# Kernel optimization log

Hardware: AMD Instinct MI355X
Metric: run time of the kernel (lower is better)

Reference implementation:

```python
import jax, jax.numpy as jnp
import numpy as np

BN_EPS = 1e-5


def _pixel_shuffle(t, r):
    # torch F.pixel_shuffle: [B, C*r^2, H, W] -> [B, C, H*r, W*r]
    B, Cr2, H, W = t.shape
    C = Cr2 // (r * r)
    t = t.reshape(B, C, r, r, H, W)
    t = t.transpose(0, 1, 4, 2, 5, 3)  # B, C, H, r, W, r
    return t.reshape(B, C, H * r, W * r)


def _upsample_bilinear(x, s):
    # F.interpolate(scale_factor=s, mode='bilinear', align_corners=False)
    B, C, H, W = x.shape

    def axis(n_in):
        n_out = n_in * s
        c = (jnp.arange(n_out, dtype=x.dtype) + 0.5) / s - 0.5
        c = jnp.clip(c, 0.0, n_in - 1)
        i0 = jnp.floor(c).astype(jnp.int32)
        i1 = jnp.minimum(i0 + 1, n_in - 1)
        w = c - i0.astype(x.dtype)
        return i0, i1, w

    y0, y1, wy = axis(H)
    x0, x1, wx = axis(W)
    rows = x[:, :, y0, :] * (1.0 - wy)[None, None, :, None] + x[:, :, y1, :] * wy[None, None, :, None]
    out = rows[:, :, :, x0] * (1.0 - wx)[None, None, None, :] + rows[:, :, :, x1] * wx[None, None, None, :]
    return out


def _grid_sample(x, grid):
    # F.grid_sample bilinear, padding_mode='zeros', align_corners=False
    # x: [B,C,H,W], grid: [B,Ho,Wo,2] with (gx, gy) in [-1,1]
    B, C, H, W = x.shape
    gx, gy = grid[..., 0], grid[..., 1]
    ix = ((gx + 1.0) * W - 1.0) * 0.5
    iy = ((gy + 1.0) * H - 1.0) * 0.5
    ix0 = jnp.floor(ix).astype(jnp.int32)
    iy0 = jnp.floor(iy).astype(jnp.int32)
    ix1, iy1 = ix0 + 1, iy0 + 1
    wx1 = ix - ix0.astype(x.dtype)
    wy1 = iy - iy0.astype(x.dtype)
    wx0, wy0 = 1.0 - wx1, 1.0 - wy1

    xf = x.reshape(B, C, H * W)

    def gather(iy_, ix_):
        valid = ((iy_ >= 0) & (iy_ < H) & (ix_ >= 0) & (ix_ < W)).astype(x.dtype)
        idx = jnp.clip(iy_, 0, H - 1) * W + jnp.clip(ix_, 0, W - 1)  # [B,Ho,Wo]
        flat = idx.reshape(B, 1, -1)
        v = jnp.take_along_axis(xf, jnp.broadcast_to(flat, (B, C, flat.shape[-1])), axis=2)
        return v.reshape(B, C, *idx.shape[1:]) * valid[:, None]

    out = (gather(iy0, ix0) * (wy0 * wx0)[:, None]
           + gather(iy0, ix1) * (wy0 * wx1)[:, None]
           + gather(iy1, ix0) * (wy1 * wx0)[:, None]
           + gather(iy1, ix1) * (wy1 * wx1)[:, None])
    return out


def _conv1x1(x, w, b=None):
    y = jnp.einsum('bchw,oc->bohw', x, w)
    if b is not None:
        y = y + b[None, :, None, None]
    return y


def _forward(x, offset_w, offset_b, mask_w, mask_b, conv_w, bn_gamma, bn_beta, bn_mean, bn_var, s):
    B, C, H, W = x.shape
    x_up = _upsample_bilinear(x, s)
    offset = _conv1x1(x, offset_w, offset_b)              # [B, 2*s*s, H, W]
    mask = jax.nn.sigmoid(_conv1x1(x, mask_w, mask_b))    # [B, s*s, H, W]
    offset = _pixel_shuffle(offset, s)                    # [B, 2, H*s, W*s]
    mask = _pixel_shuffle(mask, s)                        # [B, 1, H*s, W*s]
    Hs, Ws = H * s, W * s
    gy = jnp.linspace(-1.0, 1.0, Hs, dtype=x.dtype)
    gx = jnp.linspace(-1.0, 1.0, Ws, dtype=x.dtype)
    GX, GY = jnp.meshgrid(gx, gy)                         # 'xy': GX[h,w]=gx[w], GY[h,w]=gy[h]
    base_grid = jnp.stack((GX, GY), axis=-1)              # [Hs, Ws, 2]
    grid = base_grid[None] + offset.transpose(0, 2, 3, 1)
    sampled = _grid_sample(x_up, grid)
    out = sampled * mask
    y = _conv1x1(out, conv_w)
    y = (y - bn_mean[None, :, None, None]) * jax.lax.rsqrt(bn_var[None, :, None, None] + BN_EPS)
    y = y * bn_gamma[None, :, None, None] + bn_beta[None, :, None, None]
    return y * jax.nn.sigmoid(y)  # SiLU


def setup_inputs() -> dict:
    key = jax.random.key(0)
    ks = jax.random.split(key, 8)
    B, C, H, W, s = 16, 64, 80, 80, 2
    f = jnp.float32
    x = jax.random.normal(ks[0], (B, C, H, W), f)
    offset_w = jax.random.normal(ks[1], (2 * s * s, C), f) * 0.05
    offset_b = jax.random.normal(ks[2], (2 * s * s,), f) * 0.05
    mask_w = jax.random.normal(ks[3], (s * s, C), f) * 0.1
    mask_b = jnp.zeros((s * s,), f)
    conv_w = jax.random.normal(ks[4], (C, C), f) * (1.0 / np.sqrt(C))
    bn_gamma = jnp.ones((C,), f)
    bn_beta = jnp.zeros((C,), f)
    bn_mean = jax.random.normal(ks[5], (C,), f) * 0.1
    bn_var = jax.random.uniform(ks[6], (C,), f, 0.5, 1.5)
    return {"x": x, "offset_w": offset_w, "offset_b": offset_b, "mask_w": mask_w,
            "mask_b": mask_b, "conv_w": conv_w, "bn_gamma": bn_gamma, "bn_beta": bn_beta,
            "bn_mean": bn_mean, "bn_var": bn_var, "scale": 2}


def reference(x, offset_w, offset_b, mask_w, mask_b, conv_w, bn_gamma, bn_beta, bn_mean, bn_var, scale):
    return _forward(x, offset_w, offset_b, mask_w, mask_b, conv_w, bn_gamma, bn_beta, bn_mean, bn_var, scale)
```

## Files before the change

kernel.cpp:

```cpp
#include <hip/hip_runtime.h>

typedef unsigned short ushort_t;
typedef __attribute__((ext_vector_type(8))) short bf16x8;
typedef __attribute__((ext_vector_type(4))) float f32x4;

__device__ __forceinline__ float bf2f(ushort_t u) {
    union { unsigned int i; float f; } v; v.i = ((unsigned int)u) << 16; return v.f;
}
__device__ __forceinline__ ushort_t f2bf(float f) {
    union { float f; unsigned int i; } v; v.f = f;
    unsigned int r = v.i + 0x7FFFu + ((v.i >> 16) & 1u);
    return (ushort_t)(r >> 16);
}

#define BB 16
#define CC 64
#define HH 80
#define WW 80
#define HS 160
#define WS 160
#define HW (HH*WW)
#define HWS (HS*WS)

__global__ void prep_params(const float* __restrict__ offset_w,
                            const float* __restrict__ offset_b,
                            const float* __restrict__ mask_w,
                            const float* __restrict__ mask_b,
                            const float* __restrict__ conv_w,
                            const float* __restrict__ gamma,
                            const float* __restrict__ beta,
                            const float* __restrict__ mean,
                            const float* __restrict__ var,
                            float* __restrict__ wmat, float* __restrict__ wbias,
                            ushort_t* __restrict__ cwBf,
                            float* __restrict__ bnA, float* __restrict__ bnB) {
    int t = threadIdx.x;
    for (int i = t; i < 12 * 64; i += 256) {
        int ch = i >> 6, c = i & 63;
        wmat[i] = ch < 8 ? offset_w[ch * 64 + c] : mask_w[(ch - 8) * 64 + c];
    }
    if (t < 12) wbias[t] = t < 8 ? offset_b[t] : mask_b[t - 8];
    for (int i = t; i < 64 * 64; i += 256) cwBf[i] = f2bf(conv_w[i]);
    if (t < 64) {
        float A = gamma[t] * rsqrtf(var[t] + 1e-5f);
        bnA[t] = A;
        bnB[t] = beta[t] - mean[t] * A;
    }
}

__global__ __launch_bounds__(256) void prep_x(const float* __restrict__ x,
                                              const float* __restrict__ wmat,
                                              const float* __restrict__ wbias,
                                              ushort_t* __restrict__ xT,
                                              float* __restrict__ offs) {
    __shared__ float sX[64 * 65];
    int t = threadIdx.x;
    int tile = blockIdx.x;
    int b = tile / 100;
    int hw0 = (tile - b * 100) * 64;
#pragma unroll
    for (int k = 0; k < 16; ++k) {
        int e = k * 256 + t;
        int c = e >> 6, j = e & 63;
        sX[j * 65 + c] = x[((b * CC + c) * HW) + hw0 + j];
    }
    __syncthreads();
#pragma unroll
    for (int k = 0; k < 16; ++k) {
        int e = k * 256 + t;
        int j = e >> 6, c = e & 63;
        xT[((size_t)(b * HW) + hw0 + j) * CC + c] = f2bf(sX[j * 65 + c]);
    }
    int px = t & 63;
    int chunk = __builtin_amdgcn_readfirstlane(t >> 6);
    int ch0 = chunk * 3;
    const float* w0 = wmat + (ch0 + 0) * 64;
    const float* w1 = wmat + (ch0 + 1) * 64;
    const float* w2 = wmat + (ch0 + 2) * 64;
    float a0 = 0.f, a1 = 0.f, a2 = 0.f;
#pragma unroll 4
    for (int c = 0; c < 64; ++c) {
        float v = sX[px * 65 + c];
        a0 += v * w0[c];
        a1 += v * w1[c];
        a2 += v * w2[c];
    }
    a0 += wbias[ch0 + 0];
    a1 += wbias[ch0 + 1];
    a2 += wbias[ch0 + 2];
    if (ch0 + 0 >= 8) a0 = 1.0f / (1.0f + __expf(-a0));
    if (ch0 + 1 >= 8) a1 = 1.0f / (1.0f + __expf(-a1));
    if (ch0 + 2 >= 8) a2 = 1.0f / (1.0f + __expf(-a2));
    float* op = offs + (size_t)(b * HW + hw0 + px) * 12;
    op[ch0 + 0] = a0;
    op[ch0 + 1] = a1;
    op[ch0 + 2] = a2;
}

#define ACC3(w, k, val) { float _v = (val); \
    w[0] += (k) == 0 ? _v : 0.f; w[1] += (k) == 1 ? _v : 0.f; w[2] += (k) == 2 ? _v : 0.f; }

__device__ __forceinline__ void axis_taps(float pos, int& base, float w[3]) {
    float f = floorf(pos); int u0 = (int)f; float g1 = pos - f;
    w[0] = w[1] = w[2] = 0.f;
    bool v0 = (u0 >= 0) & (u0 < 160);
    bool v1 = (u0 + 1 >= 0) & (u0 + 1 < 160);
    float cc0 = 0.f, cc1 = 0.f; int ca0 = 0, ca1 = 0;
    if (v0) { cc0 = fminf(fmaxf((float)u0 * 0.5f - 0.25f, 0.f), 79.f); ca0 = (int)floorf(cc0); }
    if (v1) { cc1 = fminf(fmaxf((float)(u0 + 1) * 0.5f - 0.25f, 0.f), 79.f); ca1 = (int)floorf(cc1); }
    int first = v0 ? ca0 : (v1 ? ca1 : 0);
    base = min(first, 77);
    if (v0) {
        float wv = cc0 - (float)ca0; int c1 = min(ca0 + 1, 79);
        int k0 = ca0 - base, k1 = c1 - base;
        ACC3(w, k0, (1.f - g1) * (1.f - wv));
        ACC3(w, k1, (1.f - g1) * wv);
    }
    if (v1) {
        float wv = cc1 - (float)ca1; int c1 = min(ca1 + 1, 79);
        int k0 = ca1 - base, k1 = c1 - base;
        ACC3(w, k0, g1 * (1.f - wv));
        ACC3(w, k1, g1 * wv);
    }
}

__global__ __launch_bounds__(256) void dysample_main(const ushort_t* __restrict__ xT,
                                                     const float* __restrict__ offs,
                                                     const ushort_t* __restrict__ cwBf,
                                                     const float* __restrict__ bnA,
                                                     const float* __restrict__ bnB,
                                                     float* __restrict__ out) {
    __shared__ float sTap[64 * 8];
    __shared__ ushort_t S[64 * 72];
    int t = threadIdx.x;
    int lane = t & 63;
    int wave = __builtin_amdgcn_readfirstlane(t >> 6);
    int quad = lane >> 4, nrow = lane & 15;
    int b = blockIdx.y;
    int pix0 = blockIdx.x * 64;

    const ushort_t* wp = cwBf + (wave * 16 + nrow) * 64 + quad * 8;
    bf16x8 af0 = *(const bf16x8*)(wp);
    bf16x8 af1 = *(const bf16x8*)(wp + 32);
    int coutD = wave * 16 + quad * 4;
    float bnAv[4], bnBv[4];
#pragma unroll
    for (int j = 0; j < 4; ++j) { bnAv[j] = bnA[coutD + j]; bnBv[j] = bnB[coutD + j]; }

    if (t < 64) {
        int pix = pix0 + t;
        int ho = pix / WS, wo = pix - ho * WS;
        int h = ho >> 1, w = wo >> 1, r = ((ho & 1) << 1) | (wo & 1);
        const float* op = offs + (size_t)((b * HW) + h * WW + w) * 12;
        float ox = op[r], oy = op[4 + r], mk = op[8 + r];
        float ix = (float)wo * (160.0f / 159.0f) - 0.5f + 80.0f * ox;
        float iy = (float)ho * (160.0f / 159.0f) - 0.5f + 80.0f * oy;
        int cb, rb; float cw[3], rw[3];
        axis_taps(ix, cb, cw);
        axis_taps(iy, rb, rw);
        sTap[t * 8 + 0] = __int_as_float(cb | (rb << 16));
        sTap[t * 8 + 1] = cw[0]; sTap[t * 8 + 2] = cw[1]; sTap[t * 8 + 3] = cw[2];
        sTap[t * 8 + 4] = rw[0]; sTap[t * 8 + 5] = rw[1]; sTap[t * 8 + 6] = rw[2];
        sTap[t * 8 + 7] = mk;
    }
    __syncthreads();

    const ushort_t* xb = xT + (size_t)b * HW * CC;
#pragma unroll 2
    for (int i = 0; i < 16; ++i) {
        int px = wave * 16 + i;
        f32x4 t0 = *(const f32x4*)(sTap + px * 8);
        f32x4 t1 = *(const f32x4*)(sTap + px * 8 + 4);
        int bits = __float_as_int(t0.x);
        int cb = bits & 0xffff, rb = bits >> 16;
        const ushort_t* p0 = xb + (rb * WW + cb) * CC + lane;
        float acc = 0.f;
#pragma unroll
        for (int rr = 0; rr < 3; ++rr) {
            const ushort_t* pr = p0 + rr * (WW * CC);
            float v0 = bf2f(pr[0]);
            float v1 = bf2f(pr[64]);
            float v2 = bf2f(pr[128]);
            float rowa = t0.y * v0 + t0.z * v1 + t0.w * v2;
            float rwv = (rr == 0) ? t1.x : ((rr == 1) ? t1.y : t1.z);
            acc += rwv * rowa;
        }
        S[px * 72 + lane] = f2bf(acc * t1.w);
    }
    __syncthreads();

    f32x4 acc4[4];
#pragma unroll
    for (int n = 0; n < 4; ++n) acc4[n] = (f32x4){0.f, 0.f, 0.f, 0.f};
#pragma unroll
    for (int n = 0; n < 4; ++n) {
        const ushort_t* sp = S + (n * 16 + nrow) * 72 + quad * 8;
        bf16x8 b0 = *(const bf16x8*)(sp);
        bf16x8 b1 = *(const bf16x8*)(sp + 32);
        acc4[n] = __builtin_amdgcn_mfma_f32_16x16x32_bf16(af0, b0, acc4[n], 0, 0, 0);
        acc4[n] = __builtin_amdgcn_mfma_f32_16x16x32_bf16(af1, b1, acc4[n], 0, 0, 0);
    }

    size_t ob = (size_t)b * CC * HWS;
#pragma unroll
    for (int n = 0; n < 4; ++n) {
        int pix = pix0 + n * 16 + nrow;
#pragma unroll
        for (int j = 0; j < 4; ++j) {
            float y = acc4[n][j] * bnAv[j] + bnBv[j];
            float s = y / (1.0f + __expf(-y));
            out[ob + (size_t)(coutD + j) * HWS + pix] = s;
        }
    }
}

extern "C" void kernel_launch(void* const* d_in, const int* in_sizes, int n_in,
                              void* d_out, int out_size, void* d_ws, size_t ws_size,
                              hipStream_t stream) {
    const float* x        = (const float*)d_in[0];
    const float* offset_w = (const float*)d_in[1];
    const float* offset_b = (const float*)d_in[2];
    const float* mask_w   = (const float*)d_in[3];
    const float* mask_b   = (const float*)d_in[4];
    const float* conv_w   = (const float*)d_in[5];
    const float* bn_gamma = (const float*)d_in[6];
    const float* bn_beta  = (const float*)d_in[7];
    const float* bn_mean  = (const float*)d_in[8];
    const float* bn_var   = (const float*)d_in[9];

    char* ws = (char*)d_ws;
    size_t off = 0;
    ushort_t* xT   = (ushort_t*)(ws + off); off += (size_t)BB * HW * CC * 2;
    float*    offs = (float*)(ws + off);    off += (size_t)BB * HW * 12 * 4;
    ushort_t* cwBf = (ushort_t*)(ws + off); off += 64 * 64 * 2;
    float*    wmat = (float*)(ws + off);    off += 12 * 64 * 4;
    float*    wbias= (float*)(ws + off);    off += 64;
    float*    bnA  = (float*)(ws + off);    off += 64 * 4;
    float*    bnB  = (float*)(ws + off);    off += 64 * 4;

    prep_params<<<1, 256, 0, stream>>>(offset_w, offset_b, mask_w, mask_b, conv_w,
                                       bn_gamma, bn_beta, bn_mean, bn_var,
                                       wmat, wbias, cwBf, bnA, bnB);
    prep_x<<<BB * (HW / 64), 256, 0, stream>>>(x, wmat, wbias, xT, offs);
    dysample_main<<<dim3(HWS / 64, BB), 256, 0, stream>>>(xT, offs, cwBf, bnA, bnB,
                                                          (float*)d_out);
}
```

Before: 189.9 us.

## Fold parameter prep into consumer kernels and vectorize transpose loads/stores

Removes the single-block prep_params launch. Its work moves into the consumers: prep_x reads the offset and mask weights directly, and dysample_main converts conv weights to bf16 and computes the BN scale and shift per block. prep_x now uses float4 global loads and 4-wide bf16 stores for the NCHW-to-NHWC transpose, and the offset fetch in dysample_main uses vector loads. This saves a kernel launch and its serialization, at the cost of redundant per-block weight conversion and more scattered LDS writes.

```diff
diff --git a/kernel.cpp b/kernel.cpp
--- a/kernel.cpp
+++ b/kernel.cpp
@@ -2,6 +2,7 @@
 
 typedef unsigned short ushort_t;
 typedef __attribute__((ext_vector_type(8))) short bf16x8;
+typedef __attribute__((ext_vector_type(4))) unsigned short u16x4;
 typedef __attribute__((ext_vector_type(4))) float f32x4;
 
 __device__ __forceinline__ float bf2f(ushort_t u) {
@@ -12,6 +13,7 @@
     unsigned int r = v.i + 0x7FFFu + ((v.i >> 16) & 1u);
     return (ushort_t)(r >> 16);
 }
+__device__ __forceinline__ short f2bs(float f) { return (short)f2bf(f); }
 
 #define BB 16
 #define CC 64
@@ -22,35 +24,11 @@
 #define HW (HH*WW)
 #define HWS (HS*WS)
 
-__global__ void prep_params(const float* __restrict__ offset_w,
-                            const float* __restrict__ offset_b,
-                            const float* __restrict__ mask_w,
-                            const float* __restrict__ mask_b,
-                            const float* __restrict__ conv_w,
-                            const float* __restrict__ gamma,
-                            const float* __restrict__ beta,
-                            const float* __restrict__ mean,
-                            const float* __restrict__ var,
-                            float* __restrict__ wmat, float* __restrict__ wbias,
-                            ushort_t* __restrict__ cwBf,
-                            float* __restrict__ bnA, float* __restrict__ bnB) {
-    int t = threadIdx.x;
-    for (int i = t; i < 12 * 64; i += 256) {
-        int ch = i >> 6, c = i & 63;
-        wmat[i] = ch < 8 ? offset_w[ch * 64 + c] : mask_w[(ch - 8) * 64 + c];
-    }
-    if (t < 12) wbias[t] = t < 8 ? offset_b[t] : mask_b[t - 8];
-    for (int i = t; i < 64 * 64; i += 256) cwBf[i] = f2bf(conv_w[i]);
-    if (t < 64) {
-        float A = gamma[t] * rsqrtf(var[t] + 1e-5f);
-        bnA[t] = A;
-        bnB[t] = beta[t] - mean[t] * A;
-    }
-}
-
 __global__ __launch_bounds__(256) void prep_x(const float* __restrict__ x,
-                                              const float* __restrict__ wmat,
-                                              const float* __restrict__ wbias,
+                                              const float* __restrict__ offset_w,
+                                              const float* __restrict__ offset_b,
+                                              const float* __restrict__ mask_w,
+                                              const float* __restrict__ mask_b,
                                               ushort_t* __restrict__ xT,
                                               float* __restrict__ offs) {
     __shared__ float sX[64 * 65];
@@ -58,26 +36,43 @@
     int tile = blockIdx.x;
     int b = tile / 100;
     int hw0 = (tile - b * 100) * 64;
-#pragma unroll
-    for (int k = 0; k < 16; ++k) {
-        int e = k * 256 + t;
-        int c = e >> 6, j = e & 63;
-        sX[j * 65 + c] = x[((b * CC + c) * HW) + hw0 + j];
+    const float* xb = x + (size_t)b * CC * HW + hw0;
+
+#pragma unroll
+    for (int k = 0; k < 4; ++k) {
+        int idx = k * 256 + t;
+        int c = idx >> 4;
+        int j4 = (idx & 15) << 2;
+        f32x4 v = *(const f32x4*)(xb + c * HW + j4);
+        sX[(j4 + 0) * 65 + c] = v.x;
+        sX[(j4 + 1) * 65 + c] = v.y;
+        sX[(j4 + 2) * 65 + c] = v.z;
+        sX[(j4 + 3) * 65 + c] = v.w;
     }
     __syncthreads();
-#pragma unroll
-    for (int k = 0; k < 16; ++k) {
-        int e = k * 256 + t;
-        int j = e >> 6, c = e & 63;
-        xT[((size_t)(b * HW) + hw0 + j) * CC + c] = f2bf(sX[j * 65 + c]);
-    }
+
+#pragma unroll
+    for (int k = 0; k < 4; ++k) {
+        int idx = k * 256 + t;
+        int px = idx >> 4;
+        int c4 = (idx & 15) << 2;
+        u16x4 u;
+        u.x = f2bf(sX[px * 65 + c4 + 0]);
+        u.y = f2bf(sX[px * 65 + c4 + 1]);
+        u.z = f2bf(sX[px * 65 + c4 + 2]);
+        u.w = f2bf(sX[px * 65 + c4 + 3]);
+        *(u16x4*)(xT + ((size_t)(b * HW) + hw0 + px) * CC + c4) = u;
+    }
+
     int px = t & 63;
     int chunk = __builtin_amdgcn_readfirstlane(t >> 6);
     int ch0 = chunk * 3;
-    const float* w0 = wmat + (ch0 + 0) * 64;
-    const float* w1 = wmat + (ch0 + 1) * 64;
-    const float* w2 = wmat + (ch0 + 2) * 64;
-    float a0 = 0.f, a1 = 0.f, a2 = 0.f;
+    const float* w0 = (ch0 + 0) < 8 ? offset_w + (ch0 + 0) * 64 : mask_w + (ch0 - 8) * 64;
+    const float* w1 = (ch0 + 1) < 8 ? offset_w + (ch0 + 1) * 64 : mask_w + (ch0 - 7) * 64;
+    const float* w2 = (ch0 + 2) < 8 ? offset_w + (ch0 + 2) * 64 : mask_w + (ch0 - 6) * 64;
+    float a0 = (ch0 + 0) < 8 ? offset_b[ch0 + 0] : mask_b[ch0 - 8];
+    float a1 = (ch0 + 1) < 8 ? offset_b[ch0 + 1] : mask_b[ch0 - 7];
+    float a2 = (ch0 + 2) < 8 ? offset_b[ch0 + 2] : mask_b[ch0 - 6];
 #pragma unroll 4
     for (int c = 0; c < 64; ++c) {
         float v = sX[px * 65 + c];
@@ -85,9 +80,6 @@
         a1 += v * w1[c];
         a2 += v * w2[c];
     }
-    a0 += wbias[ch0 + 0];
-    a1 += wbias[ch0 + 1];
-    a2 += wbias[ch0 + 2];
     if (ch0 + 0 >= 8) a0 = 1.0f / (1.0f + __expf(-a0));
     if (ch0 + 1 >= 8) a1 = 1.0f / (1.0f + __expf(-a1));
     if (ch0 + 2 >= 8) a2 = 1.0f / (1.0f + __expf(-a2));
@@ -124,14 +116,22 @@
     }
 }
 
+__device__ __forceinline__ float pick4(f32x4 v, int r) {
+    float lo = (r & 1) ? v.y : v.x;
+    float hi = (r & 1) ? v.w : v.z;
+    return (r & 2) ? hi : lo;
+}
+
 __global__ __launch_bounds__(256) void dysample_main(const ushort_t* __restrict__ xT,
                                                      const float* __restrict__ offs,
-                                                     const ushort_t* __restrict__ cwBf,
-                                                     const float* __restrict__ bnA,
-                                                     const float* __restrict__ bnB,
+                                                     const float* __restrict__ conv_w,
+                                                     const float* __restrict__ gamma,
+                                                     const float* __restrict__ beta,
+                                                     const float* __restrict__ mean,
+                                                     const float* __restrict__ var,
                                                      float* __restrict__ out) {
-    __shared__ float sTap[64 * 8];
-    __shared__ ushort_t S[64 * 72];
+    __shared__ f32x4 sTap4[64 * 2];
+    __shared__ __align__(16) ushort_t S[64 * 72];
     int t = threadIdx.x;
     int lane = t & 63;
     int wave = __builtin_amdgcn_readfirstlane(t >> 6);
@@ -139,29 +139,40 @@
     int b = blockIdx.y;
     int pix0 = blockIdx.x * 64;
 
-    const ushort_t* wp = cwBf + (wave * 16 + nrow) * 64 + quad * 8;
-    bf16x8 af0 = *(const bf16x8*)(wp);
-    bf16x8 af1 = *(const bf16x8*)(wp + 32);
+    const float* wp = conv_w + (wave * 16 + nrow) * 64 + quad * 8;
+    f32x4 wa0 = *(const f32x4*)(wp);
+    f32x4 wa1 = *(const f32x4*)(wp + 4);
+    f32x4 wb0 = *(const f32x4*)(wp + 32);
+    f32x4 wb1 = *(const f32x4*)(wp + 36);
+    bf16x8 af0 = (bf16x8){f2bs(wa0.x), f2bs(wa0.y), f2bs(wa0.z), f2bs(wa0.w),
+                          f2bs(wa1.x), f2bs(wa1.y), f2bs(wa1.z), f2bs(wa1.w)};
+    bf16x8 af1 = (bf16x8){f2bs(wb0.x), f2bs(wb0.y), f2bs(wb0.z), f2bs(wb0.w),
+                          f2bs(wb1.x), f2bs(wb1.y), f2bs(wb1.z), f2bs(wb1.w)};
     int coutD = wave * 16 + quad * 4;
     float bnAv[4], bnBv[4];
 #pragma unroll
-    for (int j = 0; j < 4; ++j) { bnAv[j] = bnA[coutD + j]; bnBv[j] = bnB[coutD + j]; }
+    for (int j = 0; j < 4; ++j) {
+        float A = gamma[coutD + j] * rsqrtf(var[coutD + j] + 1e-5f);
+        bnAv[j] = A;
+        bnBv[j] = beta[coutD + j] - mean[coutD + j] * A;
+    }
 
     if (t < 64) {
         int pix = pix0 + t;
         int ho = pix / WS, wo = pix - ho * WS;
         int h = ho >> 1, w = wo >> 1, r = ((ho & 1) << 1) | (wo & 1);
         const float* op = offs + (size_t)((b * HW) + h * WW + w) * 12;
-        float ox = op[r], oy = op[4 + r], mk = op[8 + r];
+        f32x4 o0 = *(const f32x4*)(op);
+        f32x4 o1 = *(const f32x4*)(op + 4);
+        f32x4 o2 = *(const f32x4*)(op + 8);
+        float ox = pick4(o0, r), oy = pick4(o1, r), mk = pick4(o2, r);
         float ix = (float)wo * (160.0f / 159.0f) - 0.5f + 80.0f * ox;
         float iy = (float)ho * (160.0f / 159.0f) - 0.5f + 80.0f * oy;
         int cb, rb; float cw[3], rw[3];
         axis_taps(ix, cb, cw);
         axis_taps(iy, rb, rw);
-        sTap[t * 8 + 0] = __int_as_float(cb | (rb << 16));
-        sTap[t * 8 + 1] = cw[0]; sTap[t * 8 + 2] = cw[1]; sTap[t * 8 + 3] = cw[2];
-        sTap[t * 8 + 4] = rw[0]; sTap[t * 8 + 5] = rw[1]; sTap[t * 8 + 6] = rw[2];
-        sTap[t * 8 + 7] = mk;
+        sTap4[t * 2 + 0] = (f32x4){__int_as_float(cb | (rb << 16)), cw[0], cw[1], cw[2]};
+        sTap4[t * 2 + 1] = (f32x4){rw[0], rw[1], rw[2], mk};
     }
     __syncthreads();
 
@@ -169,8 +180,8 @@
 #pragma unroll 2
     for (int i = 0; i < 16; ++i) {
         int px = wave * 16 + i;
-        f32x4 t0 = *(const f32x4*)(sTap + px * 8);
-        f32x4 t1 = *(const f32x4*)(sTap + px * 8 + 4);
+        f32x4 t0 = sTap4[px * 2 + 0];
+        f32x4 t1 = sTap4[px * 2 + 1];
         int bits = __float_as_int(t0.x);
         int cb = bits & 0xffff, rb = bits >> 16;
         const ushort_t* p0 = xb + (rb * WW + cb) * CC + lane;
@@ -232,16 +243,10 @@
     size_t off = 0;
     ushort_t* xT   = (ushort_t*)(ws + off); off += (size_t)BB * HW * CC * 2;
     float*    offs = (float*)(ws + off);    off += (size_t)BB * HW * 12 * 4;
-    ushort_t* cwBf = (ushort_t*)(ws + off); off += 64 * 64 * 2;
-    float*    wmat = (float*)(ws + off);    off += 12 * 64 * 4;
-    float*    wbias= (float*)(ws + off);    off += 64;
-    float*    bnA  = (float*)(ws + off);    off += 64 * 4;
-    float*    bnB  = (float*)(ws + off);    off += 64 * 4;
-
-    prep_params<<<1, 256, 0, stream>>>(offset_w, offset_b, mask_w, mask_b, conv_w,
-                                       bn_gamma, bn_beta, bn_mean, bn_var,
-                                       wmat, wbias, cwBf, bnA, bnB);
-    prep_x<<<BB * (HW / 64), 256, 0, stream>>>(x, wmat, wbias, xT, offs);
-    dysample_main<<<dim3(HWS / 64, BB), 256, 0, stream>>>(xT, offs, cwBf, bnA, bnB,
-                                                          (float*)d_out);
-}
+
+    prep_x<<<BB * (HW / 64), 256, 0, stream>>>(x, offset_w, offset_b, mask_w, mask_b,
+                                               xT, offs);
+    dysample_main<<<dim3(HWS / 64, BB), 256, 0, stream>>>(xT, offs, conv_w,
+                                                          bn_gamma, bn_beta, bn_mean,
+                                                          bn_var, (float*)d_out);
+}
```

Result: slower. 194.5 us (+2.4%).
